# Performance work log

Hardware: AMD Instinct MI355X
Metric: run time of the kernel (lower is better)

## Reference

```python
import jax, jax.numpy as jnp
import numpy as np

B, N, DIM = 8, 4096, 128

def setup_inputs() -> dict:
    key = jax.random.key(0)
    ks = jax.random.split(key, 6)
    s = 1.0 / np.sqrt(DIM)
    return {
        "x": jax.random.normal(ks[0], (B, N, DIM), dtype=jnp.float32),
        "q_global": jax.random.normal(ks[1], (B, N, DIM), dtype=jnp.float32),
        "Wkv": jax.random.normal(ks[2], (DIM, 2 * DIM), dtype=jnp.float32) * s,
        "bkv": jax.random.normal(ks[3], (2 * DIM,), dtype=jnp.float32) * 0.02,
        "Wp": jax.random.normal(ks[4], (DIM, DIM), dtype=jnp.float32) * s,
        "bp": jax.random.normal(ks[5], (DIM,), dtype=jnp.float32) * 0.02,
    }

def reference(x, q_global, Wkv, bkv, Wp, bp):
    # x: [B, n, dim]; kv linear -> split into k, v (each [B, n, dim])
    kv = x @ Wkv + bkv
    k, v = jnp.split(kv, 2, axis=-1)
    dim = x.shape[-1]
    q = q_global * (1.0 / jnp.sqrt(jnp.asarray(dim, x.dtype)))
    # scores = k @ q^T : [B, n, m]; softmax over query axis m (as in source)
    scores = jnp.einsum("bnd,bmd->bnm", k, q)
    attn = jax.nn.softmax(scores, axis=-1)
    # attention @ v : contracts m against v's row index (m == n)
    out = jnp.einsum("bnm,bmd->bnd", attn, v)
    return out @ Wp + bp
```

## Files before the change

kernel.cpp:

```cpp
#include <hip/hip_runtime.h>

typedef __bf16 bf16x8 __attribute__((ext_vector_type(8)));
typedef float f32x4 __attribute__((ext_vector_type(4)));

struct alignas(16) US8 { unsigned short us[8]; };

static __device__ inline unsigned short f2bf(float f) {
  union { float f; unsigned u; } v; v.f = f;
  unsigned r = v.u + 0x7fffu + ((v.u >> 16) & 1u);
  return (unsigned short)(r >> 16);
}

#define NSEQ 4096
#define DIM 128
#define ROWS 32768
#define KH 2

#define EXPC (1.4426950408889634f * 0.08838834764831845f)

__global__ void prep_kernel(const float* __restrict__ Wkv, const float* __restrict__ Wp,
                            unsigned short* __restrict__ wkvT, unsigned short* __restrict__ wpT) {
  const int t = threadIdx.x;
  const int d = (t & 63) * 2;
  if (blockIdx.x < 64) {
    const int col = blockIdx.x * 4 + (t >> 6);
    unsigned short lo = f2bf(Wkv[d * 256 + col]);
    unsigned short hi = f2bf(Wkv[(d + 1) * 256 + col]);
    *reinterpret_cast<unsigned*>(&wkvT[col * 128 + d]) = (unsigned)lo | ((unsigned)hi << 16);
  } else {
    const int col = (blockIdx.x - 64) * 4 + (t >> 6);
    unsigned short lo = f2bf(Wp[d * 128 + col]);
    unsigned short hi = f2bf(Wp[(d + 1) * 128 + col]);
    *reinterpret_cast<unsigned*>(&wpT[col * 128 + d]) = (unsigned)lo | ((unsigned)hi << 16);
  }
}

__global__ __launch_bounds__(256, 2) void kv_kernel(
    const float* __restrict__ x, const unsigned short* __restrict__ wkvT,
    const float* __restrict__ bkv, const float* __restrict__ q,
    unsigned short* __restrict__ kout, unsigned short* __restrict__ vtout,
    unsigned short* __restrict__ qo) {
  const int tid = threadIdx.x;
  if (blockIdx.x >= 256) {
    int i = ((blockIdx.x - 256) * 256 + tid) * 8;
    const float4* p = reinterpret_cast<const float4*>(q + i);
    float4 a = p[0], b = p[1];
    US8 o;
    o.us[0]=f2bf(a.x*EXPC); o.us[1]=f2bf(a.y*EXPC); o.us[2]=f2bf(a.z*EXPC); o.us[3]=f2bf(a.w*EXPC);
    o.us[4]=f2bf(b.x*EXPC); o.us[5]=f2bf(b.y*EXPC); o.us[6]=f2bf(b.z*EXPC); o.us[7]=f2bf(b.w*EXPC);
    *reinterpret_cast<US8*>(qo + i) = o;
    return;
  }
  __shared__ __align__(16) unsigned short WT[256 * 136];
  const int wv = tid >> 6, lane = tid & 63, l16 = lane & 15, quad = lane >> 4;
  const int row0 = blockIdx.x * 128;

  for (int p = 0; p < 16; ++p) {
    int c = p * 256 + tid;
    int col = c >> 4, c16 = c & 15;
    *reinterpret_cast<US8*>(&WT[col * 136 + c16 * 8]) =
        *reinterpret_cast<const US8*>(wkvT + col * 128 + c16 * 8);
  }
  __syncthreads();

  bf16x8 afrag[2][4];
  for (int rg = 0; rg < 2; ++rg) {
    const int arow = row0 + wv * 32 + rg * 16 + l16;
    for (int s = 0; s < 4; ++s) {
      const float4* xp = reinterpret_cast<const float4*>(x + (size_t)arow * DIM + s * 32 + quad * 8);
      float4 u0 = xp[0], u1 = xp[1];
      US8 af;
      af.us[0]=f2bf(u0.x); af.us[1]=f2bf(u0.y); af.us[2]=f2bf(u0.z); af.us[3]=f2bf(u0.w);
      af.us[4]=f2bf(u1.x); af.us[5]=f2bf(u1.y); af.us[6]=f2bf(u1.z); af.us[7]=f2bf(u1.w);
      afrag[rg][s] = __builtin_bit_cast(bf16x8, af);
    }
  }
  f32x4 acc[2][16];
  for (int rg = 0; rg < 2; ++rg)
    for (int g = 0; g < 16; ++g) acc[rg][g] = f32x4{0.f, 0.f, 0.f, 0.f};
  for (int s = 0; s < 4; ++s)
    for (int g = 0; g < 16; ++g) {
      bf16x8 bfr = *reinterpret_cast<const bf16x8*>(&WT[(g * 16 + l16) * 136 + s * 32 + quad * 8]);
      acc[0][g] = __builtin_amdgcn_mfma_f32_16x16x32_bf16(afrag[0][s], bfr, acc[0][g], 0, 0, 0);
      acc[1][g] = __builtin_amdgcn_mfma_f32_16x16x32_bf16(afrag[1][s], bfr, acc[1][g], 0, 0, 0);
    }

  for (int rg = 0; rg < 2; ++rg)
    for (int g = 0; g < 8; ++g) {
      float bias = bkv[g * 16 + l16];
      for (int r = 0; r < 4; ++r) {
        int orow = row0 + wv * 32 + rg * 16 + quad * 4 + r;
        kout[(size_t)orow * DIM + g * 16 + l16] = f2bf(acc[rg][g][r] + bias);
      }
    }
  __syncthreads();
  unsigned short* LDSt = WT;
  for (int rg = 0; rg < 2; ++rg)
    for (int g = 0; g < 8; ++g) {
      float bias = bkv[128 + g * 16 + l16];
      for (int r = 0; r < 4; ++r)
        LDSt[(g * 16 + l16) * 136 + wv * 32 + rg * 16 + quad * 4 + r] = f2bf(acc[rg][g + 8][r] + bias);
    }
  __syncthreads();
  const int bb = row0 >> 12, n0 = row0 & (NSEQ - 1);
  unsigned short* vb = vtout + (size_t)bb * NSEQ * DIM;
  for (int p = 0; p < 8; ++p) {
    int c = p * 256 + tid;
    int d = c >> 4, c8 = c & 15;
    *reinterpret_cast<US8*>(vb + (size_t)d * NSEQ + n0 + c8 * 8) =
        *reinterpret_cast<const US8*>(&LDSt[d * 136 + c8 * 8]);
  }
}

__global__ __launch_bounds__(256, 2) void attn_kernel(
    const unsigned short* __restrict__ kbuf, const unsigned short* __restrict__ qbuf,
    const unsigned short* __restrict__ vtbuf,
    float* __restrict__ opart, float* __restrict__ lpart) {
  __shared__ __align__(16) unsigned short SH[27136];
  const int tid = threadIdx.x;
  const int wv = tid >> 6, lane = tid & 63, l16 = lane & 15, quad = lane >> 4;
  const int b = blockIdx.x & 7;
  const int t = blockIdx.x >> 3;
  const int q0 = (t & 31) * 128;
  const int kh = t >> 5;
  const int key0 = kh * (NSEQ / KH);
  const unsigned short* kb = kbuf + (size_t)b * NSEQ * DIM;
  const unsigned short* qb = qbuf + (size_t)b * NSEQ * DIM;
  const unsigned short* vtb = vtbuf + (size_t)b * NSEQ * DIM;

  unsigned short* Ksh  = SH;
  unsigned short* VTsh = SH + 8704;
  unsigned short* pp   = SH + 17920 + wv * 2304;

  bf16x8 afrag[2][4];
  for (int rg = 0; rg < 2; ++rg) {
    const int arow = q0 + wv * 32 + rg * 16 + l16;
    for (int s = 0; s < 4; ++s)
      afrag[rg][s] = __builtin_bit_cast(bf16x8,
          *reinterpret_cast<const US8*>(kb + (size_t)arow * DIM + s * 32 + quad * 8));
  }

  f32x4 Oacc[2][8];
  for (int rg = 0; rg < 2; ++rg)
    for (int g = 0; g < 8; ++g) Oacc[rg][g] = f32x4{0.f, 0.f, 0.f, 0.f};
  float lsum[2][4];
  for (int rg = 0; rg < 2; ++rg)
    for (int r = 0; r < 4; ++r) lsum[rg][r] = 0.f;

  for (int it = 0; it < NSEQ / KH / 64; ++it) {
    const int m0 = key0 + it * 64;
    __syncthreads();
    for (int p = 0; p < 4; ++p) {
      int c = p * 256 + tid;
      int row = c >> 4, c16 = c & 15;
      *reinterpret_cast<US8*>(&Ksh[row * 136 + c16 * 8]) =
          *reinterpret_cast<const US8*>(qb + (size_t)(m0 + row) * DIM + c16 * 8);
    }
    for (int p = 0; p < 4; ++p) {
      int c = p * 256 + tid;
      int d = c >> 3, c8 = c & 7;
      *reinterpret_cast<US8*>(&VTsh[d * 72 + c8 * 8]) =
          *reinterpret_cast<const US8*>(vtb + (size_t)d * NSEQ + m0 + c8 * 8);
    }
    __syncthreads();

    f32x4 S[2][4];
    for (int rg = 0; rg < 2; ++rg)
      for (int g = 0; g < 4; ++g) S[rg][g] = f32x4{0.f, 0.f, 0.f, 0.f};
    for (int s = 0; s < 4; ++s)
      for (int g = 0; g < 4; ++g) {
        bf16x8 bfr = *reinterpret_cast<const bf16x8*>(&Ksh[(g * 16 + l16) * 136 + s * 32 + quad * 8]);
        S[0][g] = __builtin_amdgcn_mfma_f32_16x16x32_bf16(afrag[0][s], bfr, S[0][g], 0, 0, 0);
        S[1][g] = __builtin_amdgcn_mfma_f32_16x16x32_bf16(afrag[1][s], bfr, S[1][g], 0, 0, 0);
      }

    for (int rg = 0; rg < 2; ++rg)
      for (int g = 0; g < 4; ++g)
        for (int r = 0; r < 4; ++r) {
          float pv = exp2f(S[rg][g][r]);
          unsigned u = __builtin_bit_cast(unsigned, pv) & 0xffff0000u;
          lsum[rg][r] += __builtin_bit_cast(float, u);
          pp[(rg * 16 + quad * 4 + r) * 72 + ((g ^ quad) * 16) + l16] = (unsigned short)(u >> 16);
        }

    asm volatile("s_waitcnt lgkmcnt(0)" ::: "memory");

    for (int s2 = 0; s2 < 2; ++s2) {
      const int G = ((s2 * 2 + (quad >> 1)) ^ (l16 >> 2)) * 16 + (quad & 1) * 8;
      bf16x8 pa0 = *reinterpret_cast<const bf16x8*>(&pp[l16 * 72 + G]);
      bf16x8 pa1 = *reinterpret_cast<const bf16x8*>(&pp[(16 + l16) * 72 + G]);
      for (int g = 0; g < 8; ++g) {
        bf16x8 vfr = *reinterpret_cast<const bf16x8*>(&VTsh[(g * 16 + l16) * 72 + s2 * 32 + quad * 8]);
        Oacc[0][g] = __builtin_amdgcn_mfma_f32_16x16x32_bf16(pa0, vfr, Oacc[0][g], 0, 0, 0);
        Oacc[1][g] = __builtin_amdgcn_mfma_f32_16x16x32_bf16(pa1, vfr, Oacc[1][g], 0, 0, 0);
      }
    }
  }

  for (int rg = 0; rg < 2; ++rg)
    for (int r = 0; r < 4; ++r) {
      float v = lsum[rg][r];
      for (int m = 1; m < 16; m <<= 1) v += __shfl_xor(v, m);
      lsum[rg][r] = v;
    }
  if (l16 == 0) {
    float* lp = lpart + (size_t)kh * ROWS + (size_t)b * NSEQ + q0 + wv * 32;
    for (int rg = 0; rg < 2; ++rg)
      for (int r = 0; r < 4; ++r) lp[rg * 16 + quad * 4 + r] = lsum[rg][r];
  }
  float* ob = opart + (size_t)kh * ROWS * DIM + ((size_t)b * NSEQ + q0 + wv * 32) * DIM;
  for (int rg = 0; rg < 2; ++rg)
    for (int g = 0; g < 8; ++g)
      for (int r = 0; r < 4; ++r)
        ob[(rg * 16 + quad * 4 + r) * DIM + g * 16 + l16] = Oacc[rg][g][r];
}

__global__ __launch_bounds__(256, 2) void combine_proj_kernel(
    const float* __restrict__ opart, const float* __restrict__ lpart,
    const unsigned short* __restrict__ wpT, const float* __restrict__ bp,
    float* __restrict__ out) {
  __shared__ __align__(16) unsigned short WT[128 * 136];
  const int tid = threadIdx.x;
  const int wv = tid >> 6, lane = tid & 63, l16 = lane & 15, quad = lane >> 4;
  const int row0 = blockIdx.x * 128;

  for (int p = 0; p < 8; ++p) {
    int c = p * 256 + tid;
    int col = c >> 4, c16 = c & 15;
    *reinterpret_cast<US8*>(&WT[col * 136 + c16 * 8]) =
        *reinterpret_cast<const US8*>(wpT + col * 128 + c16 * 8);
  }
  __syncthreads();

  f32x4 acc[2][8];
  for (int rg = 0; rg < 2; ++rg)
    for (int g = 0; g < 8; ++g) acc[rg][g] = f32x4{0.f, 0.f, 0.f, 0.f};
  for (int rg = 0; rg < 2; ++rg) {
    const int arow = row0 + wv * 32 + rg * 16 + l16;
    float linv = 1.f / (lpart[arow] + lpart[ROWS + arow]);
    for (int s = 0; s < 4; ++s) {
      const size_t base = (size_t)arow * DIM + s * 32 + quad * 8;
      float4 s0 = *reinterpret_cast<const float4*>(opart + base);
      float4 s1 = *reinterpret_cast<const float4*>(opart + base + 4);
      float4 u0 = *reinterpret_cast<const float4*>(opart + (size_t)ROWS * DIM + base);
      float4 u1 = *reinterpret_cast<const float4*>(opart + (size_t)ROWS * DIM + base + 4);
      US8 af;
      af.us[0]=f2bf((s0.x+u0.x)*linv); af.us[1]=f2bf((s0.y+u0.y)*linv);
      af.us[2]=f2bf((s0.z+u0.z)*linv); af.us[3]=f2bf((s0.w+u0.w)*linv);
      af.us[4]=f2bf((s1.x+u1.x)*linv); af.us[5]=f2bf((s1.y+u1.y)*linv);
      af.us[6]=f2bf((s1.z+u1.z)*linv); af.us[7]=f2bf((s1.w+u1.w)*linv);
      bf16x8 a = __builtin_bit_cast(bf16x8, af);
      for (int g = 0; g < 8; ++g) {
        bf16x8 bfr = *reinterpret_cast<const bf16x8*>(&WT[(g * 16 + l16) * 136 + s * 32 + quad * 8]);
        acc[rg][g] = __builtin_amdgcn_mfma_f32_16x16x32_bf16(a, bfr, acc[rg][g], 0, 0, 0);
      }
    }
  }
  for (int rg = 0; rg < 2; ++rg)
    for (int g = 0; g < 8; ++g) {
      float bias = bp[g * 16 + l16];
      for (int r = 0; r < 4; ++r) {
        int orow = row0 + wv * 32 + rg * 16 + quad * 4 + r;
        out[(size_t)orow * DIM + g * 16 + l16] = acc[rg][g][r] + bias;
      }
    }
}

extern "C" void kernel_launch(void* const* d_in, const int* in_sizes, int n_in,
                              void* d_out, int out_size, void* d_ws, size_t ws_size,
                              hipStream_t stream) {
  (void)in_sizes; (void)n_in; (void)out_size; (void)ws_size;
  const float* x   = (const float*)d_in[0];
  const float* qg  = (const float*)d_in[1];
  const float* Wkv = (const float*)d_in[2];
  const float* bkv = (const float*)d_in[3];
  const float* Wp  = (const float*)d_in[4];
  const float* bp  = (const float*)d_in[5];
  float* out = (float*)d_out;

  unsigned short* qbf  = (unsigned short*)d_ws;
  unsigned short* kbf  = qbf + (size_t)ROWS * DIM;
  unsigned short* vtbf = kbf + (size_t)ROWS * DIM;
  unsigned short* wkvT = vtbf + (size_t)ROWS * DIM;
  unsigned short* wpT  = wkvT + 256 * 128;
  float* lpart = (float*)(wpT + 128 * 128);
  float* opart = lpart + (size_t)KH * ROWS;

  hipLaunchKernelGGL(prep_kernel, dim3(96), dim3(256), 0, stream, Wkv, Wp, wkvT, wpT);
  hipLaunchKernelGGL(kv_kernel, dim3(256 + 2048), dim3(256), 0, stream,
                     x, wkvT, bkv, qg, kbf, vtbf, qbf);
  hipLaunchKernelGGL(attn_kernel, dim3(8 * 32 * KH), dim3(256), 0, stream, kbf, qbf, vtbf, opart, lpart);
  hipLaunchKernelGGL(combine_proj_kernel, dim3(ROWS / 128), dim3(256), 0, stream, opart, lpart, wpT, bp, out);
}
```

Before: 196.4 us.

## Restructure attention with 32x32 MFMA, register-resident P, and pre-tiled Q/V layouts

```diff
diff --git a/kernel.cpp b/kernel.cpp
--- a/kernel.cpp
+++ b/kernel.cpp
@@ -2,6 +2,7 @@
 
 typedef __bf16 bf16x8 __attribute__((ext_vector_type(8)));
 typedef float f32x4 __attribute__((ext_vector_type(4)));
+typedef float f32x16 __attribute__((ext_vector_type(16)));
 
 struct alignas(16) US8 { unsigned short us[8]; };
 
@@ -9,6 +10,12 @@
   union { float f; unsigned u; } v; v.f = f;
   unsigned r = v.u + 0x7fffu + ((v.u >> 16) & 1u);
   return (unsigned short)(r >> 16);
+}
+
+static __device__ inline void gload16(const unsigned short* g, unsigned short* l) {
+  __builtin_amdgcn_global_load_lds(
+      (const __attribute__((address_space(1))) void*)g,
+      (__attribute__((address_space(3))) void*)l, 16, 0, 0);
 }
 
 #define NSEQ 4096
@@ -48,7 +55,9 @@
     US8 o;
     o.us[0]=f2bf(a.x*EXPC); o.us[1]=f2bf(a.y*EXPC); o.us[2]=f2bf(a.z*EXPC); o.us[3]=f2bf(a.w*EXPC);
     o.us[4]=f2bf(b.x*EXPC); o.us[5]=f2bf(b.y*EXPC); o.us[6]=f2bf(b.z*EXPC); o.us[7]=f2bf(b.w*EXPC);
-    *reinterpret_cast<US8*>(qo + i) = o;
+    int row = i >> 7, d0 = i & 127;
+    int bb = row >> 12, n = row & (NSEQ - 1), tile = n >> 6, l = n & 63, kc = d0 >> 3;
+    *reinterpret_cast<US8*>(qo + (size_t)bb * NSEQ * DIM + tile * 8192 + kc * 512 + l * 8) = o;
     return;
   }
   __shared__ __align__(16) unsigned short WT[256 * 136];
@@ -99,120 +108,111 @@
     for (int g = 0; g < 8; ++g) {
       float bias = bkv[128 + g * 16 + l16];
       for (int r = 0; r < 4; ++r)
-        LDSt[(g * 16 + l16) * 136 + wv * 32 + rg * 16 + quad * 4 + r] = f2bf(acc[rg][g + 8][r] + bias);
-    }
-  __syncthreads();
-  const int bb = row0 >> 12, n0 = row0 & (NSEQ - 1);
-  unsigned short* vb = vtout + (size_t)bb * NSEQ * DIM;
+        LDSt[(g * 16 + l16) * 140 + wv * 32 + rg * 16 + quad * 4 + r] = f2bf(acc[rg][g + 8][r] + bias);
+    }
+  __syncthreads();
+  const int bb = row0 >> 12, tilebase = (row0 & (NSEQ - 1)) >> 6;
+  unsigned short* vbo = vtout + (size_t)bb * NSEQ * DIM;
   for (int p = 0; p < 8; ++p) {
     int c = p * 256 + tid;
-    int d = c >> 4, c8 = c & 15;
-    *reinterpret_cast<US8*>(vb + (size_t)d * NSEQ + n0 + c8 * 8) =
-        *reinterpret_cast<const US8*>(&LDSt[d * 136 + c8 * 8]);
+    int tl = c >> 10, u = c & 1023, idx = u >> 6, l = u & 63;
+    int mg = idx >> 1, dh = idx & 1, d = dh * 64 + l;
+    int nb = tl * 64 + (mg >> 1) * 16 + (mg & 1) * 4;
+    uint2 lo = *reinterpret_cast<const uint2*>(&LDSt[d * 140 + nb]);
+    uint2 hi = *reinterpret_cast<const uint2*>(&LDSt[d * 140 + nb + 8]);
+    uint4 o{lo.x, lo.y, hi.x, hi.y};
+    *reinterpret_cast<uint4*>(vbo + (size_t)(tilebase + tl) * 8192 + idx * 512 + l * 8) = o;
   }
 }
 
 __global__ __launch_bounds__(256, 2) void attn_kernel(
-    const unsigned short* __restrict__ kbuf, const unsigned short* __restrict__ qbuf,
-    const unsigned short* __restrict__ vtbuf,
+    const unsigned short* __restrict__ kbuf, const unsigned short* __restrict__ qblk,
+    const unsigned short* __restrict__ vblk,
     float* __restrict__ opart, float* __restrict__ lpart) {
-  __shared__ __align__(16) unsigned short SH[27136];
+  __shared__ __align__(16) unsigned short SH[16384];
+  unsigned short* Ksh = SH;
+  unsigned short* Vsh = SH + 8192;
   const int tid = threadIdx.x;
-  const int wv = tid >> 6, lane = tid & 63, l16 = lane & 15, quad = lane >> 4;
+  const int wv = tid >> 6, lane = tid & 63, l32 = lane & 31, h = lane >> 5;
   const int b = blockIdx.x & 7;
   const int t = blockIdx.x >> 3;
   const int q0 = (t & 31) * 128;
   const int kh = t >> 5;
   const int key0 = kh * (NSEQ / KH);
   const unsigned short* kb = kbuf + (size_t)b * NSEQ * DIM;
-  const unsigned short* qb = qbuf + (size_t)b * NSEQ * DIM;
-  const unsigned short* vtb = vtbuf + (size_t)b * NSEQ * DIM;
-
-  unsigned short* Ksh  = SH;
-  unsigned short* VTsh = SH + 8704;
-  unsigned short* pp   = SH + 17920 + wv * 2304;
-
-  bf16x8 afrag[2][4];
-  for (int rg = 0; rg < 2; ++rg) {
-    const int arow = q0 + wv * 32 + rg * 16 + l16;
-    for (int s = 0; s < 4; ++s)
-      afrag[rg][s] = __builtin_bit_cast(bf16x8,
-          *reinterpret_cast<const US8*>(kb + (size_t)arow * DIM + s * 32 + quad * 8));
-  }
-
-  f32x4 Oacc[2][8];
-  for (int rg = 0; rg < 2; ++rg)
-    for (int g = 0; g < 8; ++g) Oacc[rg][g] = f32x4{0.f, 0.f, 0.f, 0.f};
-  float lsum[2][4];
-  for (int rg = 0; rg < 2; ++rg)
-    for (int r = 0; r < 4; ++r) lsum[rg][r] = 0.f;
+  const unsigned short* qb = qblk + (size_t)b * NSEQ * DIM;
+  const unsigned short* vb = vblk + (size_t)b * NSEQ * DIM;
+
+  bf16x8 kfrag[8];
+  for (int ks = 0; ks < 8; ++ks)
+    kfrag[ks] = __builtin_bit_cast(bf16x8, *reinterpret_cast<const US8*>(
+        kb + (size_t)(q0 + wv * 32 + l32) * DIM + ks * 16 + h * 8));
+
+  f32x16 Oacc[4];
+  for (int dt = 0; dt < 4; ++dt)
+    for (int i = 0; i < 16; ++i) Oacc[dt][i] = 0.f;
+  float lsum = 0.f;
 
   for (int it = 0; it < NSEQ / KH / 64; ++it) {
-    const int m0 = key0 + it * 64;
+    const int tile = (key0 + it * 64) >> 6;
     __syncthreads();
-    for (int p = 0; p < 4; ++p) {
-      int c = p * 256 + tid;
-      int row = c >> 4, c16 = c & 15;
-      *reinterpret_cast<US8*>(&Ksh[row * 136 + c16 * 8]) =
-          *reinterpret_cast<const US8*>(qb + (size_t)(m0 + row) * DIM + c16 * 8);
-    }
-    for (int p = 0; p < 4; ++p) {
-      int c = p * 256 + tid;
-      int d = c >> 3, c8 = c & 7;
-      *reinterpret_cast<US8*>(&VTsh[d * 72 + c8 * 8]) =
-          *reinterpret_cast<const US8*>(vtb + (size_t)d * NSEQ + m0 + c8 * 8);
+    for (int c = 0; c < 8; ++c) {
+      int idx = wv * 8 + c;
+      if (idx < 16)
+        gload16(qb + (size_t)tile * 8192 + idx * 512 + lane * 8, &Ksh[idx * 512]);
+      else
+        gload16(vb + (size_t)tile * 8192 + (idx - 16) * 512 + lane * 8, &Vsh[(idx - 16) * 512]);
     }
     __syncthreads();
 
-    f32x4 S[2][4];
-    for (int rg = 0; rg < 2; ++rg)
-      for (int g = 0; g < 4; ++g) S[rg][g] = f32x4{0.f, 0.f, 0.f, 0.f};
-    for (int s = 0; s < 4; ++s)
-      for (int g = 0; g < 4; ++g) {
-        bf16x8 bfr = *reinterpret_cast<const bf16x8*>(&Ksh[(g * 16 + l16) * 136 + s * 32 + quad * 8]);
-        S[0][g] = __builtin_amdgcn_mfma_f32_16x16x32_bf16(afrag[0][s], bfr, S[0][g], 0, 0, 0);
-        S[1][g] = __builtin_amdgcn_mfma_f32_16x16x32_bf16(afrag[1][s], bfr, S[1][g], 0, 0, 0);
-      }
-
-    for (int rg = 0; rg < 2; ++rg)
-      for (int g = 0; g < 4; ++g)
-        for (int r = 0; r < 4; ++r) {
-          float pv = exp2f(S[rg][g][r]);
-          unsigned u = __builtin_bit_cast(unsigned, pv) & 0xffff0000u;
-          lsum[rg][r] += __builtin_bit_cast(float, u);
-          pp[(rg * 16 + quad * 4 + r) * 72 + ((g ^ quad) * 16) + l16] = (unsigned short)(u >> 16);
+    f32x16 S0, S1;
+    for (int i = 0; i < 16; ++i) { S0[i] = 0.f; S1[i] = 0.f; }
+    for (int ks = 0; ks < 8; ++ks) {
+      const unsigned short* kc = &Ksh[(ks * 2 + h) * 512];
+      bf16x8 a0 = *reinterpret_cast<const bf16x8*>(&kc[l32 * 8]);
+      bf16x8 a1 = *reinterpret_cast<const bf16x8*>(&kc[(32 + l32) * 8]);
+      S0 = __builtin_amdgcn_mfma_f32_32x32x16_bf16(a0, kfrag[ks], S0, 0, 0, 0);
+      S1 = __builtin_amdgcn_mfma_f32_32x32x16_bf16(a1, kfrag[ks], S1, 0, 0, 0);
+    }
+
+    bf16x8 pf[2][2];
+    for (int T = 0; T < 2; ++T) {
+      unsigned pk[8];
+      for (int i2 = 0; i2 < 8; ++i2) {
+        float e0 = exp2f(T ? S1[i2 * 2] : S0[i2 * 2]);
+        float e1 = exp2f(T ? S1[i2 * 2 + 1] : S0[i2 * 2 + 1]);
+        unsigned u0 = __builtin_bit_cast(unsigned, e0) & 0xffff0000u;
+        unsigned u1 = __builtin_bit_cast(unsigned, e1) & 0xffff0000u;
+        lsum += __builtin_bit_cast(float, u0) + __builtin_bit_cast(float, u1);
+        pk[i2] = (u0 >> 16) | u1;
+      }
+      pf[T][0] = __builtin_bit_cast(bf16x8, uint4{pk[0], pk[1], pk[2], pk[3]});
+      pf[T][1] = __builtin_bit_cast(bf16x8, uint4{pk[4], pk[5], pk[6], pk[7]});
+    }
+
+    for (int T = 0; T < 2; ++T)
+      for (int s = 0; s < 2; ++s) {
+        const int mg = 4 * T + 2 * s + h;
+        for (int dt = 0; dt < 4; ++dt) {
+          bf16x8 bv = *reinterpret_cast<const bf16x8*>(
+              &Vsh[(mg * 2 + (dt >> 1)) * 512 + ((dt & 1) * 32 + l32) * 8]);
+          Oacc[dt] = __builtin_amdgcn_mfma_f32_32x32x16_bf16(pf[T][s], bv, Oacc[dt], 0, 0, 0);
         }
-
-    asm volatile("s_waitcnt lgkmcnt(0)" ::: "memory");
-
-    for (int s2 = 0; s2 < 2; ++s2) {
-      const int G = ((s2 * 2 + (quad >> 1)) ^ (l16 >> 2)) * 16 + (quad & 1) * 8;
-      bf16x8 pa0 = *reinterpret_cast<const bf16x8*>(&pp[l16 * 72 + G]);
-      bf16x8 pa1 = *reinterpret_cast<const bf16x8*>(&pp[(16 + l16) * 72 + G]);
-      for (int g = 0; g < 8; ++g) {
-        bf16x8 vfr = *reinterpret_cast<const bf16x8*>(&VTsh[(g * 16 + l16) * 72 + s2 * 32 + quad * 8]);
-        Oacc[0][g] = __builtin_amdgcn_mfma_f32_16x16x32_bf16(pa0, vfr, Oacc[0][g], 0, 0, 0);
-        Oacc[1][g] = __builtin_amdgcn_mfma_f32_16x16x32_bf16(pa1, vfr, Oacc[1][g], 0, 0, 0);
-      }
-    }
-  }
-
-  for (int rg = 0; rg < 2; ++rg)
-    for (int r = 0; r < 4; ++r) {
-      float v = lsum[rg][r];
-      for (int m = 1; m < 16; m <<= 1) v += __shfl_xor(v, m);
-      lsum[rg][r] = v;
-    }
-  if (l16 == 0) {
-    float* lp = lpart + (size_t)kh * ROWS + (size_t)b * NSEQ + q0 + wv * 32;
-    for (int rg = 0; rg < 2; ++rg)
-      for (int r = 0; r < 4; ++r) lp[rg * 16 + quad * 4 + r] = lsum[rg][r];
+      }
+  }
+
+  {
+    float v = lsum;
+    v += __shfl_xor(v, 32);
+    if (lane < 32)
+      lpart[(size_t)kh * ROWS + (size_t)b * NSEQ + q0 + wv * 32 + l32] = v;
   }
   float* ob = opart + (size_t)kh * ROWS * DIM + ((size_t)b * NSEQ + q0 + wv * 32) * DIM;
-  for (int rg = 0; rg < 2; ++rg)
-    for (int g = 0; g < 8; ++g)
-      for (int r = 0; r < 4; ++r)
-        ob[(rg * 16 + quad * 4 + r) * DIM + g * 16 + l16] = Oacc[rg][g][r];
+  for (int dt = 0; dt < 4; ++dt)
+    for (int i = 0; i < 16; ++i) {
+      int n = (i & 3) + 8 * (i >> 2) + 4 * h;
+      ob[n * DIM + dt * 32 + l32] = Oacc[dt][i];
+    }
 }
 
 __global__ __launch_bounds__(256, 2) void combine_proj_kernel(
```

Result: faster. 190.2 us (-3.1%).
